# Performance work log

Hardware: AMD Instinct MI355X
Metric: run time of the kernel (lower is better)

The kernel has to match this reference:

```python
import jax, jax.numpy as jnp
import numpy as np

D_MODEL = 1024
NUM_HEADS = 16
HEAD_DIM = D_MODEL // NUM_HEADS


def setup_inputs() -> dict:
    key = jax.random.key(0)
    k_x, k_qkv, k_proj, k_pb = jax.random.split(key, 4)
    x = jax.random.normal(k_x, (4, 2048, D_MODEL), dtype=jnp.float32)
    s = 1.0 / np.sqrt(D_MODEL)
    W_qkv = jax.random.uniform(k_qkv, (D_MODEL, 3 * D_MODEL), minval=-s, maxval=s, dtype=jnp.float32)
    W_proj = jax.random.uniform(k_proj, (D_MODEL, D_MODEL), minval=-s, maxval=s, dtype=jnp.float32)
    b_proj = jax.random.uniform(k_pb, (D_MODEL,), minval=-s, maxval=s, dtype=jnp.float32)
    return {"x": x, "W_qkv": W_qkv, "W_proj": W_proj, "b_proj": b_proj}


def reference(x, W_qkv, W_proj, b_proj):
    B, N, D = x.shape
    H, Hd = NUM_HEADS, HEAD_DIM
    scale = Hd ** -0.5
    qkv = jnp.einsum('bnd,de->bne', x, W_qkv)  # (B, N, 3D), no bias (qkv_bias=False)
    qkv = qkv.reshape(B, N, 3, H, Hd).transpose(2, 0, 3, 1, 4)  # (3, B, H, N, Hd)
    q, k, v = qkv[0], qkv[1], qkv[2]
    attn = jnp.einsum('bhqd,bhkd->bhqk', q, k) * scale  # (B, H, N, N)
    attn = jax.nn.softmax(attn, axis=-1)
    out = jnp.einsum('bhqk,bhkd->bhqd', attn, v)  # (B, H, N, Hd)
    out = out.transpose(0, 2, 1, 3).reshape(B, N, D)
    return jnp.einsum('bnd,de->bne', out, W_proj) + b_proj
```

## Files before the change

kernel.cpp:

```cpp
#include <hip/hip_runtime.h>


#define DEV __device__ __forceinline__

typedef __attribute__((ext_vector_type(8))) short bf16x8;
typedef __attribute__((ext_vector_type(4))) float f32x4;
typedef __attribute__((ext_vector_type(2))) __bf16 bf16x2v;

DEV unsigned short f2b(float f) {
  union { float f; unsigned u; } x; x.f = f;
  unsigned r = (x.u + 0x7FFFu + ((x.u >> 16) & 1u)) >> 16;
  return (unsigned short)r;
}

DEV unsigned pkbf(float a, float b) {
  bf16x2v v; v[0] = (__bf16)a; v[1] = (__bf16)b;
  union { bf16x2v v; unsigned u; } x; x.v = v; return x.u;
}

DEV void gload16(const void* g, void* l) {
  __builtin_amdgcn_global_load_lds((const __attribute__((address_space(1))) void*)g,
                                   (__attribute__((address_space(3))) void*)l,
                                   16, 0, 0);
}

__global__ void k_cvt(const float* __restrict__ in, unsigned short* __restrict__ out) {
  int i = (blockIdx.x * 256 + threadIdx.x) * 4;
  float4 v = *(const float4*)&in[i];
  *(uint2*)&out[i] = make_uint2(pkbf(v.x, v.y), pkbf(v.z, v.w));
}

__global__ void k_wt(const float* __restrict__ W, unsigned short* __restrict__ Wt,
                     int Nw, int K) {
  __shared__ float t[64][65];
  const int k0 = blockIdx.y * 64, n0 = blockIdx.x * 64;
  const int tx = threadIdx.x, ty = threadIdx.y;
#pragma unroll
  for (int i = 0; i < 16; ++i) {
    int r = i * 4 + ty;
    t[r][tx] = W[(size_t)(k0 + r) * Nw + n0 + tx];
  }
  __syncthreads();
#pragma unroll
  for (int i = 0; i < 16; ++i) {
    int r = i * 4 + ty;
    Wt[(size_t)(n0 + r) * K + k0 + tx] = f2b(t[tx][r]);
  }
}

__global__ void k_vt(const unsigned short* __restrict__ qkv, unsigned short* __restrict__ vt) {
  __shared__ unsigned short t[64][68];
  const int bh = blockIdx.y;
  const int b = bh >> 4, h = bh & 15;
  const int n0 = blockIdx.x * 64;
  const int tx = threadIdx.x, ty = threadIdx.y;
#pragma unroll
  for (int i = 0; i < 16; ++i) {
    int r = i * 4 + ty;
    t[r][tx] = qkv[(size_t)(b * 2048 + n0 + r) * 3072 + 2048 + h * 64 + tx];
  }
  __syncthreads();
#pragma unroll
  for (int i = 0; i < 16; ++i) {
    int d = i * 4 + ty;
    vt[(size_t)(bh * 64 + d) * 2048 + n0 + tx] = t[tx][d];
  }
}

template <bool PROJ>
__global__ __launch_bounds__(256, 2) void gemm_bt(
    const unsigned short* __restrict__ A, const unsigned short* __restrict__ Bt,
    unsigned short* __restrict__ outB, float* __restrict__ outF,
    const float* __restrict__ bias, int M, int N, int K) {
  __shared__ unsigned short Al[128 * 32];
  __shared__ unsigned short Bl[128 * 32];
  const int tid = threadIdx.x;
  const int lane = tid & 63;
  const int wv = tid >> 6;
  const int m0 = blockIdx.y * 128;
  const int n0 = blockIdx.x * 128;
  const int wrow = (wv >> 1) * 64;
  const int wcol = (wv & 1) * 64;

  f32x4 acc[4][4];
#pragma unroll
  for (int i = 0; i < 4; ++i)
#pragma unroll
    for (int j = 0; j < 4; ++j) acc[i][j] = (f32x4){0.f, 0.f, 0.f, 0.f};

  const int lr = lane >> 2;
  const int lk = (lane & 3) * 8;
  const int fr = lane & 15;
  const int fg = (lane >> 4) * 8;

  const unsigned short* gA = A + (size_t)(m0 + wv * 32 + lr) * K + lk;
  const unsigned short* gB = Bt + (size_t)(n0 + wv * 32 + lr) * K + lk;
  unsigned short* lA0 = &Al[(wv * 2 + 0) * 512];
  unsigned short* lA1 = &Al[(wv * 2 + 1) * 512];
  unsigned short* lB0 = &Bl[(wv * 2 + 0) * 512];
  unsigned short* lB1 = &Bl[(wv * 2 + 1) * 512];

  const int nk = K >> 5;
  for (int kt = 0; kt < nk; ++kt) {
    const int k0 = kt << 5;
    gload16(gA + k0, lA0);
    gload16(gA + k0 + (size_t)16 * K, lA1);
    gload16(gB + k0, lB0);
    gload16(gB + k0 + (size_t)16 * K, lB1);
    __syncthreads();
    bf16x8 af[4], bfv[4];
#pragma unroll
    for (int i = 0; i < 4; ++i) af[i] = *(const bf16x8*)&Al[(wrow + i * 16 + fr) * 32 + fg];
#pragma unroll
    for (int j = 0; j < 4; ++j) bfv[j] = *(const bf16x8*)&Bl[(wcol + j * 16 + fr) * 32 + fg];
#pragma unroll
    for (int i = 0; i < 4; ++i)
#pragma unroll
      for (int j = 0; j < 4; ++j)
        acc[i][j] = __builtin_amdgcn_mfma_f32_16x16x32_bf16(af[i], bfv[j], acc[i][j], 0, 0, 0);
    __syncthreads();
  }

  const int rg = (lane >> 4) * 4;
#pragma unroll
  for (int i = 0; i < 4; ++i) {
#pragma unroll
    for (int j = 0; j < 4; ++j) {
      const int col = n0 + wcol + j * 16 + fr;
#pragma unroll
      for (int r = 0; r < 4; ++r) {
        const int row = m0 + wrow + i * 16 + rg + r;
        if (PROJ)
          outF[(size_t)row * N + col] = acc[i][j][r] + bias[col];
        else
          outB[(size_t)row * N + col] = f2b(acc[i][j][r]);
      }
    }
  }
}

__global__ __launch_bounds__(256, 3) void attn_k(
    const unsigned short* __restrict__ qkv, const unsigned short* __restrict__ vt,
    unsigned short* __restrict__ ao) {
  __shared__ unsigned short Kl[2][64 * 64];
  __shared__ unsigned short Vl[2][64 * 64];
  __shared__ unsigned short Pl[4][32 * 72];
  const int tid = threadIdx.x;
  const int lane = tid & 63;
  const int wv = tid >> 6;
  const int bh = blockIdx.x;
  const int b = bh >> 4, h = bh & 15;
  const int q0 = blockIdx.y * 128 + wv * 32;
  const int fr = lane & 15;
  const int hi = lane >> 4;
  const int g8 = hi * 8;
  const int g4 = hi * 4;
  const int fx = fr & 7;
  const float CSC = 0.125f * 1.44269504f;
  const float THR = 4.0f;

  const int sr = lane >> 3;
  const int sc = ((lane & 7) ^ (sr & 7)) * 8;
  const unsigned short* gK =
      qkv + (size_t)(b * 2048 + wv * 16 + sr) * 3072 + 1024 + h * 64 + sc;
  const unsigned short* gV =
      vt + ((size_t)bh * 64 + wv * 16 + sr) * 2048 + sc;

  bf16x8 bq[2][2];
#pragma unroll
  for (int qt = 0; qt < 2; ++qt)
#pragma unroll
    for (int ks = 0; ks < 2; ++ks)
      bq[qt][ks] = *(const bf16x8*)&qkv[(size_t)(b * 2048 + q0 + qt * 16 + fr) * 3072 +
                                        h * 64 + ks * 32 + g8];

  f32x4 acc[4][2];
#pragma unroll
  for (int i = 0; i < 4; ++i)
#pragma unroll
    for (int j = 0; j < 2; ++j) acc[i][j] = (f32x4){0.f, 0.f, 0.f, 0.f};
  float m[2] = {-1e30f, -1e30f};
  float l[2] = {0.f, 0.f};

  auto STAGE = [&](int buf, int tt) {
#pragma unroll
    for (int seg = 0; seg < 2; ++seg) {
      gload16(gK + (size_t)(tt * 64 + seg * 8) * 3072, &Kl[buf][(wv * 16 + seg * 8) * 64]);
      gload16(gV + (size_t)(seg * 8) * 2048 + tt * 64, &Vl[buf][(wv * 16 + seg * 8) * 64]);
    }
  };

  int cur = 0;
  STAGE(0, 0);
  __syncthreads();

  for (int tt = 0; tt < 32; ++tt) {
    if (tt < 31) STAGE(cur ^ 1, tt + 1);
    const unsigned short* Kb = &Kl[cur][0];
    const unsigned short* Vb = &Vl[cur][0];

    f32x4 st[4][2];
    __builtin_amdgcn_s_setprio(1);
#pragma unroll
    for (int kk = 0; kk < 4; ++kk) {
      bf16x8 ak0 = *(const bf16x8*)&Kb[(kk * 16 + fr) * 64 + ((hi ^ fx) * 8)];
      bf16x8 ak1 = *(const bf16x8*)&Kb[(kk * 16 + fr) * 64 + (((4 + hi) ^ fx) * 8)];
#pragma unroll
      for (int qt = 0; qt < 2; ++qt) {
        f32x4 z = (f32x4){0.f, 0.f, 0.f, 0.f};
        z = __builtin_amdgcn_mfma_f32_16x16x32_bf16(ak0, bq[qt][0], z, 0, 0, 0);
        st[kk][qt] = __builtin_amdgcn_mfma_f32_16x16x32_bf16(ak1, bq[qt][1], z, 0, 0, 0);
      }
    }
    __builtin_amdgcn_s_setprio(0);

#pragma unroll
    for (int qt = 0; qt < 2; ++qt) {
      float lm = st[0][qt][0];
#pragma unroll
      for (int kk = 0; kk < 4; ++kk)
#pragma unroll
        for (int r = 0; r < 4; ++r) lm = fmaxf(lm, st[kk][qt][r]);
      const float lmc = lm * CSC;
      if (!__all(lmc <= m[qt] + THR)) {
        float tm = lmc;
        tm = fmaxf(tm, __shfl_xor(tm, 16, 64));
        tm = fmaxf(tm, __shfl_xor(tm, 32, 64));
        const float mnew = fmaxf(m[qt], tm);
        const float corr = exp2f(m[qt] - mnew);
        m[qt] = mnew;
        l[qt] *= corr;
#pragma unroll
        for (int dt = 0; dt < 4; ++dt) {
          acc[dt][qt][0] *= corr; acc[dt][qt][1] *= corr;
          acc[dt][qt][2] *= corr; acc[dt][qt][3] *= corr;
        }
      }
      const float mq = m[qt];
      float p[16];
      float sum = 0.f;
#pragma unroll
      for (int kk = 0; kk < 4; ++kk)
#pragma unroll
        for (int r = 0; r < 4; ++r) {
          p[kk * 4 + r] = exp2f(__builtin_fmaf(st[kk][qt][r], CSC, -mq));
          sum += p[kk * 4 + r];
        }
      l[qt] += sum;
      const int prow = (qt * 16 + fr) * 72;
#pragma unroll
      for (int kk = 0; kk < 4; ++kk)
        *(uint2*)&Pl[wv][prow + kk * 16 + g4] =
            make_uint2(pkbf(p[kk * 4 + 0], p[kk * 4 + 1]), pkbf(p[kk * 4 + 2], p[kk * 4 + 3]));
    }

#pragma unroll
    for (int ks2 = 0; ks2 < 2; ++ks2) {
      bf16x8 bp0 = *(const bf16x8*)&Pl[wv][(0 * 16 + fr) * 72 + ks2 * 32 + g8];
      bf16x8 bp1 = *(const bf16x8*)&Pl[wv][(1 * 16 + fr) * 72 + ks2 * 32 + g8];
      __builtin_amdgcn_s_setprio(1);
#pragma unroll
      for (int dt = 0; dt < 4; ++dt) {
        bf16x8 av = *(const bf16x8*)&Vb[(dt * 16 + fr) * 64 + (((ks2 * 4 + hi) ^ fx) * 8)];
        acc[dt][0] = __builtin_amdgcn_mfma_f32_16x16x32_bf16(av, bp0, acc[dt][0], 0, 0, 0);
        acc[dt][1] = __builtin_amdgcn_mfma_f32_16x16x32_bf16(av, bp1, acc[dt][1], 0, 0, 0);
      }
      __builtin_amdgcn_s_setprio(0);
    }

    __syncthreads();
    cur ^= 1;
  }

#pragma unroll
  for (int qt = 0; qt < 2; ++qt) {
    float lf = l[qt];
    lf += __shfl_xor(lf, 16, 64);
    lf += __shfl_xor(lf, 32, 64);
    const float inv = 1.0f / lf;
#pragma unroll
    for (int dt = 0; dt < 4; ++dt) {
      uint2 o = make_uint2(pkbf(acc[dt][qt][0] * inv, acc[dt][qt][1] * inv),
                           pkbf(acc[dt][qt][2] * inv, acc[dt][qt][3] * inv));
      *(uint2*)&ao[(size_t)(b * 2048 + q0 + qt * 16 + fr) * 1024 + h * 64 + dt * 16 + g4] = o;
    }
  }
}

extern "C" void kernel_launch(void* const* d_in, const int* in_sizes, int n_in,
                              void* d_out, int out_size, void* d_ws, size_t ws_size,
                              hipStream_t stream) {
  const float* x     = (const float*)d_in[0];
  const float* wqkv  = (const float*)d_in[1];
  const float* wproj = (const float*)d_in[2];
  const float* bproj = (const float*)d_in[3];
  float* out = (float*)d_out;
  char* ws = (char*)d_ws;

  unsigned short* xb     = (unsigned short*)(ws + 0);
  unsigned short* wqkvT  = (unsigned short*)(ws + 16777216);
  unsigned short* wprojT = (unsigned short*)(ws + 23068672);
  unsigned short* qkv    = (unsigned short*)(ws + 25165824);
  unsigned short* vt     = (unsigned short*)(ws + 75497472);
  unsigned short* ao     = (unsigned short*)(ws + 92274688);

  k_cvt<<<8192, 256, 0, stream>>>(x, xb);
  k_wt<<<dim3(48, 16), dim3(64, 4), 0, stream>>>(wqkv, wqkvT, 3072, 1024);
  k_wt<<<dim3(16, 16), dim3(64, 4), 0, stream>>>(wproj, wprojT, 1024, 1024);
  gemm_bt<false><<<dim3(24, 64), 256, 0, stream>>>(xb, wqkvT, qkv, nullptr, nullptr,
                                                   8192, 3072, 1024);
  k_vt<<<dim3(32, 64), dim3(64, 4), 0, stream>>>(qkv, vt);
  attn_k<<<dim3(64, 16), 256, 0, stream>>>(qkv, vt, ao);
  gemm_bt<true><<<dim3(8, 64), 256, 0, stream>>>(ao, wprojT, nullptr, out, bproj,
                                                 8192, 1024, 1024);
}
```

Before: 332.3 us.

## Compute softmax row sums via MFMA with ones vector and swizzle attention grid

The attention kernel now accumulates the softmax denominator with an extra MFMA that multiplies the bf16 P tile by a vector of ones, replacing the per-lane scalar sum and the final cross-lane shuffle reduction. The rescale branch is merged for both query tiles, and the max and exp steps use vector elementwise builtins. The grid is flattened to 1D with a swizzle that spreads consecutive blocks across different (batch, head) pairs, which may change L2 locality for K/V. The denominator now sums bf16-rounded probabilities, which keeps it consistent with the numerator at the cost of two extra MFMAs per K tile.

```diff
diff --git a/kernel.cpp b/kernel.cpp
--- a/kernel.cpp
+++ b/kernel.cpp
@@ -148,9 +148,11 @@
   const int tid = threadIdx.x;
   const int lane = tid & 63;
   const int wv = tid >> 6;
-  const int bh = blockIdx.x;
+  const int id = blockIdx.x;
+  const int swz = (id & 7) * (1024 >> 3) + (id >> 3);
+  const int bh = swz >> 4;
   const int b = bh >> 4, h = bh & 15;
-  const int q0 = blockIdx.y * 128 + wv * 32;
+  const int q0 = (swz & 15) * 128 + wv * 32;
   const int fr = lane & 15;
   const int hi = lane >> 4;
   const int g8 = hi * 8;
@@ -174,13 +176,19 @@
       bq[qt][ks] = *(const bf16x8*)&qkv[(size_t)(b * 2048 + q0 + qt * 16 + fr) * 3072 +
                                         h * 64 + ks * 32 + g8];
 
+  bf16x8 vones;
+#pragma unroll
+  for (int j = 0; j < 8; ++j) vones[j] = (short)0x3F80;
+
   f32x4 acc[4][2];
+  f32x4 acc_l[2];
 #pragma unroll
   for (int i = 0; i < 4; ++i)
 #pragma unroll
     for (int j = 0; j < 2; ++j) acc[i][j] = (f32x4){0.f, 0.f, 0.f, 0.f};
+  acc_l[0] = (f32x4){0.f, 0.f, 0.f, 0.f};
+  acc_l[1] = (f32x4){0.f, 0.f, 0.f, 0.f};
   float m[2] = {-1e30f, -1e30f};
-  float l[2] = {0.f, 0.f};
 
   auto STAGE = [&](int buf, int tt) {
 #pragma unroll
@@ -193,6 +201,8 @@
   int cur = 0;
   STAGE(0, 0);
   __syncthreads();
+
+  const f32x4 csc4 = (f32x4){CSC, CSC, CSC, CSC};
 
   for (int tt = 0; tt < 32; ++tt) {
     if (tt < 31) STAGE(cur ^ 1, tt + 1);
@@ -214,44 +224,42 @@
     }
     __builtin_amdgcn_s_setprio(0);
 
-#pragma unroll
-    for (int qt = 0; qt < 2; ++qt) {
-      float lm = st[0][qt][0];
-#pragma unroll
-      for (int kk = 0; kk < 4; ++kk)
-#pragma unroll
-        for (int r = 0; r < 4; ++r) lm = fmaxf(lm, st[kk][qt][r]);
-      const float lmc = lm * CSC;
-      if (!__all(lmc <= m[qt] + THR)) {
-        float tm = lmc;
+    f32x4 t0 = __builtin_elementwise_max(st[0][0], st[1][0]);
+    t0 = __builtin_elementwise_max(t0, st[2][0]);
+    t0 = __builtin_elementwise_max(t0, st[3][0]);
+    f32x4 t1 = __builtin_elementwise_max(st[0][1], st[1][1]);
+    t1 = __builtin_elementwise_max(t1, st[2][1]);
+    t1 = __builtin_elementwise_max(t1, st[3][1]);
+    const float c0 = fmaxf(fmaxf(t0[0], t0[1]), fmaxf(t0[2], t0[3])) * CSC;
+    const float c1 = fmaxf(fmaxf(t1[0], t1[1]), fmaxf(t1[2], t1[3])) * CSC;
+
+    if (!__all(c0 <= m[0] + THR && c1 <= m[1] + THR)) {
+      const float cc[2] = {c0, c1};
+#pragma unroll
+      for (int qt = 0; qt < 2; ++qt) {
+        float tm = cc[qt];
         tm = fmaxf(tm, __shfl_xor(tm, 16, 64));
         tm = fmaxf(tm, __shfl_xor(tm, 32, 64));
         const float mnew = fmaxf(m[qt], tm);
         const float corr = exp2f(m[qt] - mnew);
         m[qt] = mnew;
-        l[qt] *= corr;
-#pragma unroll
-        for (int dt = 0; dt < 4; ++dt) {
-          acc[dt][qt][0] *= corr; acc[dt][qt][1] *= corr;
-          acc[dt][qt][2] *= corr; acc[dt][qt][3] *= corr;
-        }
-      }
+        acc_l[qt][0] *= corr;
+#pragma unroll
+        for (int dt = 0; dt < 4; ++dt) acc[dt][qt] *= corr;
+      }
+    }
+
+#pragma unroll
+    for (int qt = 0; qt < 2; ++qt) {
       const float mq = m[qt];
-      float p[16];
-      float sum = 0.f;
-#pragma unroll
-      for (int kk = 0; kk < 4; ++kk)
-#pragma unroll
-        for (int r = 0; r < 4; ++r) {
-          p[kk * 4 + r] = exp2f(__builtin_fmaf(st[kk][qt][r], CSC, -mq));
-          sum += p[kk * 4 + r];
-        }
-      l[qt] += sum;
+      const f32x4 mq4 = (f32x4){-mq, -mq, -mq, -mq};
       const int prow = (qt * 16 + fr) * 72;
 #pragma unroll
-      for (int kk = 0; kk < 4; ++kk)
+      for (int kk = 0; kk < 4; ++kk) {
+        f32x4 e = __builtin_elementwise_fma(st[kk][qt], csc4, mq4);
         *(uint2*)&Pl[wv][prow + kk * 16 + g4] =
-            make_uint2(pkbf(p[kk * 4 + 0], p[kk * 4 + 1]), pkbf(p[kk * 4 + 2], p[kk * 4 + 3]));
+            make_uint2(pkbf(exp2f(e[0]), exp2f(e[1])), pkbf(exp2f(e[2]), exp2f(e[3])));
+      }
     }
 
 #pragma unroll
@@ -265,6 +273,8 @@
         acc[dt][0] = __builtin_amdgcn_mfma_f32_16x16x32_bf16(av, bp0, acc[dt][0], 0, 0, 0);
         acc[dt][1] = __builtin_amdgcn_mfma_f32_16x16x32_bf16(av, bp1, acc[dt][1], 0, 0, 0);
       }
+      acc_l[0] = __builtin_amdgcn_mfma_f32_16x16x32_bf16(vones, bp0, acc_l[0], 0, 0, 0);
+      acc_l[1] = __builtin_amdgcn_mfma_f32_16x16x32_bf16(vones, bp1, acc_l[1], 0, 0, 0);
       __builtin_amdgcn_s_setprio(0);
     }
 
@@ -274,10 +284,7 @@
 
 #pragma unroll
   for (int qt = 0; qt < 2; ++qt) {
-    float lf = l[qt];
-    lf += __shfl_xor(lf, 16, 64);
-    lf += __shfl_xor(lf, 32, 64);
-    const float inv = 1.0f / lf;
+    const float inv = 1.0f / acc_l[qt][0];
 #pragma unroll
     for (int dt = 0; dt < 4; ++dt) {
       uint2 o = make_uint2(pkbf(acc[dt][qt][0] * inv, acc[dt][qt][1] * inv),
@@ -310,7 +317,7 @@
   gemm_bt<false><<<dim3(24, 64), 256, 0, stream>>>(xb, wqkvT, qkv, nullptr, nullptr,
                                                    8192, 3072, 1024);
   k_vt<<<dim3(32, 64), dim3(64, 4), 0, stream>>>(qkv, vt);
-  attn_k<<<dim3(64, 16), 256, 0, stream>>>(qkv, vt, ao);
+  attn_k<<<1024, 256, 0, stream>>>(qkv, vt, ao);
   gemm_bt<true><<<dim3(8, 64), 256, 0, stream>>>(ao, wprojT, nullptr, out, bproj,
                                                  8192, 1024, 1024);
 }
```

Measured after the change: 321.0 us. -3.4%, faster.
